# Optimization experiments

Hardware: AMD Instinct MI355X
Metric: run time of the kernel (lower is better)

Reference implementation:

```python
import jax, jax.numpy as jnp
import numpy as np

PAD_TOKEN_ID = 0
EPS = 1e-12  # torch F.normalize eps

B_Q, L_Q = 64, 32
B_D, L_D = 512, 256
HID, OUT = 768, 128
VOCAB = 30522


def setup_inputs() -> dict:
    key = jax.random.key(0)
    k1, k2, k3, k4, k5 = jax.random.split(key, 5)
    return {
        "q_hidden": jax.random.normal(k1, (B_Q, L_Q, HID), dtype=jnp.float32),
        "d_hidden": jax.random.normal(k2, (B_D, L_D, HID), dtype=jnp.float32),
        "d_input_ids": jax.random.randint(k3, (B_D, L_D), 0, VOCAB, dtype=jnp.int32),
        "skiplist": jax.random.randint(k4, (64,), 0, VOCAB, dtype=jnp.int32),
        "W": jax.random.normal(k5, (OUT, HID), dtype=jnp.float32) * (HID ** -0.5),
    }


def _l2norm(x):
    n = jnp.sqrt(jnp.sum(x * x, axis=-1, keepdims=True))
    return x / jnp.maximum(n, EPS)


def reference(q_hidden, d_hidden, d_input_ids, skiplist, W):
    # query(): linear proj + L2 normalize      (B_q, L_q, F)
    Q = _l2norm(jnp.einsum("blh,fh->blf", q_hidden, W))
    # doc(): linear proj + L2 normalize + mask (B_d, L_d, F)
    D = _l2norm(jnp.einsum("blh,fh->blf", d_hidden, W))
    is_pad = d_input_ids == PAD_TOKEN_ID
    is_punct = jnp.any(d_input_ids[..., None] == skiplist, axis=-1)
    d_mask = (~is_pad) & (~is_punct)                     # (B_d, L_d)
    D = D * d_mask[..., None].astype(D.dtype)
    # forward(): reshape to (B, N, L, F) with B = min(B_q, B_d)
    B = min(q_hidden.shape[0], d_hidden.shape[0])
    Qr = Q.reshape(B, -1, L_Q, OUT)                      # (B, 1, L_q, F)
    Dr = D.reshape(B, -1, L_D, OUT)                      # (B, N_p, L_d, F)
    Mr = d_mask.reshape(B, -1, L_D)                      # (B, N_p, L_d)
    # similarity(): cosine MaxSim, Q @ D^T with broadcast over N_p
    sim = jnp.einsum("bqf,bndf->bnqd", Qr[:, 0], Dr)     # (B, N_p, L_q, L_d)
    sim = jnp.where(Mr[:, :, None, :], sim, -jnp.inf)
    sms = jnp.max(sim, axis=-1).mean(axis=-1)            # (B, N_p)
    return sms
```

## Files before the change

### kernel.cpp

```cpp
#include <hip/hip_runtime.h>
#include <stdint.h>

typedef float  f32x4 __attribute__((ext_vector_type(4)));
typedef short  s16x8 __attribute__((ext_vector_type(8)));
typedef unsigned int u32;
typedef unsigned short u16;
typedef unsigned int u32x4 __attribute__((ext_vector_type(4)));

#define HID 768
#define OUTF 128
#define LQ 32
#define LD 256

__device__ __forceinline__ u32 pk_rna(float lo, float hi) {
    u32 a = __builtin_bit_cast(u32, lo) + 0x8000u;
    u32 b = __builtin_bit_cast(u32, hi) + 0x8000u;
    return __builtin_amdgcn_perm(b, a, 0x07060302u);
}
__device__ __forceinline__ u16 f2bf(float x) {
    return (u16)((__builtin_bit_cast(u32, x) + 0x8000u) >> 16);
}
__device__ __forceinline__ s16x8 cvt8(f32x4 lo, f32x4 hi) {
    union { u32 u[4]; s16x8 v; } ua;
    ua.u[0] = pk_rna(lo[0], lo[1]);
    ua.u[1] = pk_rna(lo[2], lo[3]);
    ua.u[2] = pk_rna(hi[0], hi[1]);
    ua.u[3] = pk_rna(hi[2], hi[3]);
    return ua.v;
}

__global__ __launch_bounds__(256) void wconv(const float* __restrict__ W,
                                             u32* __restrict__ Wb3d) {
    int t = blockIdx.x * 256 + threadIdx.x;
    int j2   = t & 3;
    int lane = (t >> 2) & 63;
    int cf   = (t >> 8) & 7;
    int kk   = t >> 11;
    int l15 = lane & 15, g4 = lane >> 4;
    int f = cf * 16 + l15;
    int k = kk * 32 + g4 * 8 + j2 * 2;
    const float* src = W + (size_t)f * HID + k;
    Wb3d[t] = pk_rna(src[0], src[1]);
}

__global__ __launch_bounds__(256) void qproj(const float* __restrict__ qh,
                                             const u16* __restrict__ Wb3,
                                             u16* __restrict__ Qb) {
    const int b = blockIdx.x;
    const int tid = threadIdx.x;
    const int w = tid >> 6, lane = tid & 63, g = lane >> 4, l15 = lane & 15;

    f32x4 acc[2][2] = {};
    const float* A0 = qh + ((size_t)b * LQ + l15) * HID + g * 8;
    const float* A1 = A0 + 16 * HID;
    const u16* Bp = Wb3 + w * 1024 + lane * 8;

    for (int kk = 0; kk < 24; ++kk) {
        f32x4 x0 = *(const f32x4*)A0;
        f32x4 x1 = *(const f32x4*)(A0 + 4);
        f32x4 y0 = *(const f32x4*)A1;
        f32x4 y1 = *(const f32x4*)(A1 + 4);
        s16x8 b0 = *(const s16x8*)(Bp);
        s16x8 b1 = *(const s16x8*)(Bp + 512);
        s16x8 a0 = cvt8(x0, x1);
        s16x8 a1 = cvt8(y0, y1);
        acc[0][0] = __builtin_amdgcn_mfma_f32_16x16x32_bf16(a0, b0, acc[0][0], 0, 0, 0);
        acc[0][1] = __builtin_amdgcn_mfma_f32_16x16x32_bf16(a0, b1, acc[0][1], 0, 0, 0);
        acc[1][0] = __builtin_amdgcn_mfma_f32_16x16x32_bf16(a1, b0, acc[1][0], 0, 0, 0);
        acc[1][1] = __builtin_amdgcn_mfma_f32_16x16x32_bf16(a1, b1, acc[1][1], 0, 0, 0);
        A0 += 32; A1 += 32; Bp += 4096;
    }

    __shared__ float part[4][32];
    __shared__ float invl[32];
#pragma unroll
    for (int rf = 0; rf < 2; ++rf)
#pragma unroll
        for (int reg = 0; reg < 4; ++reg) {
            float ss = acc[rf][0][reg] * acc[rf][0][reg] + acc[rf][1][reg] * acc[rf][1][reg];
            ss += __shfl_xor(ss, 1); ss += __shfl_xor(ss, 2);
            ss += __shfl_xor(ss, 4); ss += __shfl_xor(ss, 8);
            if (l15 == 0) part[w][rf * 16 + g * 4 + reg] = ss;
        }
    __syncthreads();
    if (tid < 32) {
        float ss = part[0][tid] + part[1][tid] + part[2][tid] + part[3][tid];
        invl[tid] = 1.f / fmaxf(sqrtf(ss), 1e-12f);
    }
    __syncthreads();
#pragma unroll
    for (int rf = 0; rf < 2; ++rf)
#pragma unroll
        for (int cf = 0; cf < 2; ++cf)
#pragma unroll
            for (int reg = 0; reg < 4; ++reg) {
                int q = rf * 16 + g * 4 + reg;
                int f = w * 32 + cf * 16 + l15;
                Qb[(size_t)b * LQ * OUTF + q * OUTF + f] = f2bf(acc[rf][cf][reg] * invl[q]);
            }
}

__global__ __launch_bounds__(512, 2) void dmax(const float* __restrict__ dh,
                                               const int* __restrict__ ids,
                                               const int* __restrict__ skiplist,
                                               const u16* __restrict__ Wb3,
                                               const u16* __restrict__ Qb,
                                               float* __restrict__ out) {
    const int bid = blockIdx.x;
    const int tid = threadIdx.x;
    const int w = tid >> 6, lane = tid & 63, g4 = lane >> 4, l15 = lane & 15;
    const int qh_ = w >> 2;

    __shared__ __align__(16) u16 stg[3][12288];
    __shared__ __align__(16) u16 outb[2][2048];
    __shared__ __align__(16) float nrm[2][16][8];
    __shared__ float wsum[8];
    __shared__ int ms[512];
    __shared__ int sk[64];

#define PADOF(v) (((v) / 192) * 1536 + (((((v) % 192)) * 8) ^ ((((v) / 192) & 7) << 4)))
    const int pad0 = PADOF(2 * tid), pad1 = PADOF(2 * tid + 1024), pad2 = PADOF(2 * tid + 2048);

    const int swz = (l15 & 7) << 4, sw45 = swz & 48, sw6 = swz & 64;
    const int aoffE = l15 * 1536 + ((g4 * 16) ^ sw45) + sw6;
    const int aoffO = l15 * 1536 + ((g4 * 16) ^ sw45) + 64 - sw6;
    const int doffE = l15 * 256 + ((g4 * 16) ^ sw45) + sw6;
    const int doffO = l15 * 256 + ((g4 * 16) ^ sw45) + 64 - sw6;

    f32x4 LA0, LA1, LA2, LA3, LA4, LA5, LB0, LB1, LB2, LB3, LB4, LB5,
          LC0, LC1, LC2, LC3, LC4, LC5;
    s16x8 Qr0, Qr1, Qr2, Qr3;
    float rmaxH[4] = {-INFINITY, -INFINITY, -INFINITY, -INFINITY};

#define SLABBASE(sab) ((const char*)dh + (size_t)(bid + (((sab) >> 4) << 8)) * 786432 \
                       + (size_t)((sab) & 15) * 49152)

#define LISSUE(sab, S) { const char* gb_ = SLABBASE(sab) + 32 * tid; \
    S##0 = *(const f32x4*)(gb_);          S##1 = *(const f32x4*)(gb_ + 16); \
    S##2 = *(const f32x4*)(gb_ + 16384);  S##3 = *(const f32x4*)(gb_ + 16400); \
    S##4 = *(const f32x4*)(gb_ + 32768);  S##5 = *(const f32x4*)(gb_ + 32784); }

#define WSTORE(P, S) { char* sb_ = (char*)&stg[P][0]; u32x4 q_; \
    q_[0] = pk_rna(S##0[0], S##0[1]); q_[1] = pk_rna(S##0[2], S##0[3]); \
    q_[2] = pk_rna(S##1[0], S##1[1]); q_[3] = pk_rna(S##1[2], S##1[3]); \
    *(u32x4*)(sb_ + pad0) = q_; \
    q_[0] = pk_rna(S##2[0], S##2[1]); q_[1] = pk_rna(S##2[2], S##2[3]); \
    q_[2] = pk_rna(S##3[0], S##3[1]); q_[3] = pk_rna(S##3[2], S##3[3]); \
    *(u32x4*)(sb_ + pad1) = q_; \
    q_[0] = pk_rna(S##4[0], S##4[1]); q_[1] = pk_rna(S##4[2], S##4[3]); \
    q_[2] = pk_rna(S##5[0], S##5[1]); q_[3] = pk_rna(S##5[2], S##5[3]); \
    *(u32x4*)(sb_ + pad2) = q_; }

#define QLOAD(doc_) { const u16* qp_ = Qb + (size_t)((bid + (doc_) * 256) >> 3) * 4096 \
                      + (qh_ * 16 + l15) * 128 + g4 * 8; \
    Qr0 = *(const s16x8*)(qp_);      Qr1 = *(const s16x8*)(qp_ + 32); \
    Qr2 = *(const s16x8*)(qp_ + 64); Qr3 = *(const s16x8*)(qp_ + 96); }

#define GEMMN(P, s_) { \
    const char* Ab_ = (const char*)&stg[P][0]; \
    u16* ob_ = &outb[(s_) & 1][0]; \
    f32x4 ac0_ = {}, ac1_ = {}; \
    _Pragma("unroll") for (int kkp = 0; kkp < 12; ++kkp) { \
        s16x8 ae_ = *(const s16x8*)(Ab_ + aoffE + kkp * 128); \
        s16x8 ao_ = *(const s16x8*)(Ab_ + aoffO + kkp * 128); \
        ac0_ = __builtin_amdgcn_mfma_f32_16x16x32_bf16(ae_, Bf[2 * kkp],     ac0_, 0, 0, 0); \
        ac1_ = __builtin_amdgcn_mfma_f32_16x16x32_bf16(ao_, Bf[2 * kkp + 1], ac1_, 0, 0, 0); \
    } \
    f32x4 aG_ = ac0_ + ac1_; \
    _Pragma("unroll") for (int rg = 0; rg < 4; ++rg) { \
        float ss_ = aG_[rg] * aG_[rg]; \
        ss_ += __shfl_xor(ss_, 1); ss_ += __shfl_xor(ss_, 2); \
        ss_ += __shfl_xor(ss_, 4); ss_ += __shfl_xor(ss_, 8); \
        if (l15 == 0) nrm[(s_) & 1][g4 * 4 + rg][w] = ss_; \
        int dr_ = g4 * 4 + rg; \
        int of_ = (dr_ * 256 + (w * 16 + l15) * 2) ^ ((dr_ & 7) << 4); \
        *(u16*)((char*)ob_ + of_) = f2bf(aG_[rg]); \
    } }

#define TAIL(sb) { \
    if ((w & 3) == 0) { \
        const char* Db_ = (const char*)&outb[(sb) & 1][0]; \
        s16x8 d0_ = *(const s16x8*)(Db_ + doffE); \
        s16x8 d1_ = *(const s16x8*)(Db_ + doffO); \
        s16x8 d2_ = *(const s16x8*)(Db_ + doffE + 128); \
        s16x8 d3_ = *(const s16x8*)(Db_ + doffO + 128); \
        f32x4 s2_ = {}; \
        s2_ = __builtin_amdgcn_mfma_f32_16x16x32_bf16(Qr0, d0_, s2_, 0, 0, 0); \
        s2_ = __builtin_amdgcn_mfma_f32_16x16x32_bf16(Qr1, d1_, s2_, 0, 0, 0); \
        s2_ = __builtin_amdgcn_mfma_f32_16x16x32_bf16(Qr2, d2_, s2_, 0, 0, 0); \
        s2_ = __builtin_amdgcn_mfma_f32_16x16x32_bf16(Qr3, d3_, s2_, 0, 0, 0); \
        f32x4 n0_ = *(const f32x4*)&nrm[(sb) & 1][l15][0]; \
        f32x4 n1_ = *(const f32x4*)&nrm[(sb) & 1][l15][4]; \
        float ssv_ = (n0_[0] + n0_[1] + n0_[2] + n0_[3]) \
                   + (n1_[0] + n1_[1] + n1_[2] + n1_[3]); \
        float inv_ = 1.f / fmaxf(sqrtf(ssv_), 1e-12f); \
        int keep_ = ms[(((sb) >> 4) << 8) + (((sb) & 15) << 4) + l15]; \
        _Pragma("unroll") for (int rg = 0; rg < 4; ++rg) { \
            float v_ = keep_ ? s2_[rg] * inv_ : -INFINITY; \
            rmaxH[rg] = fmaxf(rmaxH[rg], v_); } \
    } \
    if (((sb) & 15) == 15) { \
        if ((w & 3) == 0) { \
            float ps_ = 0.f; \
            _Pragma("unroll") for (int rg = 0; rg < 4; ++rg) { \
                float v_ = rmaxH[rg]; \
                v_ = fmaxf(v_, __shfl_xor(v_, 1)); v_ = fmaxf(v_, __shfl_xor(v_, 2)); \
                v_ = fmaxf(v_, __shfl_xor(v_, 4)); v_ = fmaxf(v_, __shfl_xor(v_, 8)); \
                ps_ += v_; rmaxH[rg] = -INFINITY; } \
            ps_ += __shfl_xor(ps_, 16); ps_ += __shfl_xor(ps_, 32); \
            if (lane == 0) wsum[w] = ps_; \
            if ((sb) == 15) { QLOAD(1); } \
        } \
        asm volatile("s_waitcnt lgkmcnt(0)" ::: "memory"); \
        __builtin_amdgcn_s_barrier(); \
        if (tid == 0) out[bid + (((sb) >> 4) << 8)] = (wsum[0] + wsum[4]) * (1.f / 32.f); \
    } }

#define SLABSTEP(s_, PG_, PW_, RN_, RW_, doIssue_, doWr_) { \
    if (doIssue_) LISSUE((s_) + 3, RN_); \
    GEMMN(PG_, s_); \
    if (doWr_) WSTORE(PW_, RW_); \
    asm volatile("s_waitcnt lgkmcnt(0)" ::: "memory"); \
    __builtin_amdgcn_s_barrier(); \
    TAIL(s_); }

    LISSUE(0, LA);
    LISSUE(1, LB);
    LISSUE(2, LC);

    s16x8 Bf[24];
#pragma unroll
    for (int kk = 0; kk < 24; ++kk)
        Bf[kk] = *(const s16x8*)(Wb3 + (size_t)(kk * 8 + w) * 512 + lane * 8);

    if (tid < 64) sk[tid] = skiplist[tid];
    asm volatile("s_waitcnt lgkmcnt(0)" ::: "memory");
    __builtin_amdgcn_s_barrier();
    {
        int d_ = tid >> 8, r_ = tid & 255;
        int id_ = ids[(size_t)(bid + d_ * 256) * 256 + r_];
        int keep_ = (id_ != 0);
#pragma unroll
        for (int j = 0; j < 64; ++j) keep_ &= (id_ != sk[j]);
        ms[tid] = keep_;
    }
    WSTORE(0, LA);
    if ((w & 3) == 0) { QLOAD(0); }
    asm volatile("s_waitcnt lgkmcnt(0)" ::: "memory");
    __builtin_amdgcn_s_barrier();

    for (int j = 0; j < 10; ++j) {
        const int s0 = 3 * j;
        SLABSTEP(s0,     0, 1, LA, LB, true,        true);
        SLABSTEP(s0 + 1, 1, 2, LB, LC, true,        true);
        SLABSTEP(s0 + 2, 2, 0, LC, LA, s0 + 5 < 32, true);
    }
    SLABSTEP(30, 0, 1, LA, LB, false, true);
    SLABSTEP(31, 1, 2, LB, LC, false, false);
}

extern "C" void kernel_launch(void* const* d_in, const int* in_sizes, int n_in,
                              void* d_out, int out_size, void* d_ws, size_t ws_size,
                              hipStream_t stream) {
    const float* q_hidden = (const float*)d_in[0];
    const float* d_hidden = (const float*)d_in[1];
    const int*   d_ids    = (const int*)d_in[2];
    const int*   skiplist = (const int*)d_in[3];
    const float* W        = (const float*)d_in[4];
    float* out = (float*)d_out;

    u16* Wb3 = (u16*)d_ws;
    u16* Qb  = (u16*)((char*)d_ws + 256 * 1024);

    wconv<<<192, 256, 0, stream>>>(W, (u32*)Wb3);
    qproj<<<64, 256, 0, stream>>>(q_hidden, Wb3, Qb);
    dmax<<<256, 512, 0, stream>>>(d_hidden, d_ids, skiplist, Wb3, Qb, out);
}
```

Measured before the change: 102.5 us.

## Specialize warps: only six warps stage doc slabs, tail warps reload Q per slab

Global-to-LDS staging of each document slab now runs on six of the eight warps, each loading eight vectors instead of six. Warps 0 and 4 do no staging and handle the MaxSim tail. The persistent Q register fragments are dropped and Q is reloaded from global memory inside every tail step. The aim is to cut register pressure and free the tail warps from staging work so the tail overlaps better with the loads. In exchange the staging load is uneven across warps and each tail step issues extra global loads for Q.

```diff
diff --git a/kernel.cpp b/kernel.cpp
--- a/kernel.cpp
+++ b/kernel.cpp
@@ -109,7 +109,9 @@
     const int bid = blockIdx.x;
     const int tid = threadIdx.x;
     const int w = tid >> 6, lane = tid & 63, g4 = lane >> 4, l15 = lane & 15;
-    const int qh_ = w >> 2;
+    const bool stg_w = (w != 0) && (w != 4);
+    const int sw = (w < 4) ? (w - 1) : (w - 2);
+    const int st = sw * 64 + lane;
 
     __shared__ __align__(16) u16 stg[3][12288];
     __shared__ __align__(16) u16 outb[2][2048];
@@ -119,7 +121,8 @@
     __shared__ int sk[64];
 
 #define PADOF(v) (((v) / 192) * 1536 + (((((v) % 192)) * 8) ^ ((((v) / 192) & 7) << 4)))
-    const int pad0 = PADOF(2 * tid), pad1 = PADOF(2 * tid + 1024), pad2 = PADOF(2 * tid + 2048);
+    const int pd0 = PADOF(2 * st), pd1 = PADOF(2 * st + 768),
+              pd2 = PADOF(2 * st + 1536), pd3 = PADOF(2 * st + 2304);
 
     const int swz = (l15 & 7) << 4, sw45 = swz & 48, sw6 = swz & 64;
     const int aoffE = l15 * 1536 + ((g4 * 16) ^ sw45) + sw6;
@@ -127,34 +130,33 @@
     const int doffE = l15 * 256 + ((g4 * 16) ^ sw45) + sw6;
     const int doffO = l15 * 256 + ((g4 * 16) ^ sw45) + 64 - sw6;
 
-    f32x4 LA0, LA1, LA2, LA3, LA4, LA5, LB0, LB1, LB2, LB3, LB4, LB5,
-          LC0, LC1, LC2, LC3, LC4, LC5;
-    s16x8 Qr0, Qr1, Qr2, Qr3;
+    f32x4 LA0, LA1, LA2, LA3, LA4, LA5, LA6, LA7,
+          LB0, LB1, LB2, LB3, LB4, LB5, LB6, LB7,
+          LC0, LC1, LC2, LC3, LC4, LC5, LC6, LC7;
     float rmaxH[4] = {-INFINITY, -INFINITY, -INFINITY, -INFINITY};
 
 #define SLABBASE(sab) ((const char*)dh + (size_t)(bid + (((sab) >> 4) << 8)) * 786432 \
                        + (size_t)((sab) & 15) * 49152)
 
-#define LISSUE(sab, S) { const char* gb_ = SLABBASE(sab) + 32 * tid; \
+#define LISSUE(sab, S) { const char* gb_ = SLABBASE(sab) + 32 * st; \
     S##0 = *(const f32x4*)(gb_);          S##1 = *(const f32x4*)(gb_ + 16); \
-    S##2 = *(const f32x4*)(gb_ + 16384);  S##3 = *(const f32x4*)(gb_ + 16400); \
-    S##4 = *(const f32x4*)(gb_ + 32768);  S##5 = *(const f32x4*)(gb_ + 32784); }
+    S##2 = *(const f32x4*)(gb_ + 12288);  S##3 = *(const f32x4*)(gb_ + 12304); \
+    S##4 = *(const f32x4*)(gb_ + 24576);  S##5 = *(const f32x4*)(gb_ + 24592); \
+    S##6 = *(const f32x4*)(gb_ + 36864);  S##7 = *(const f32x4*)(gb_ + 36880); }
 
 #define WSTORE(P, S) { char* sb_ = (char*)&stg[P][0]; u32x4 q_; \
     q_[0] = pk_rna(S##0[0], S##0[1]); q_[1] = pk_rna(S##0[2], S##0[3]); \
     q_[2] = pk_rna(S##1[0], S##1[1]); q_[3] = pk_rna(S##1[2], S##1[3]); \
-    *(u32x4*)(sb_ + pad0) = q_; \
+    *(u32x4*)(sb_ + pd0) = q_; \
     q_[0] = pk_rna(S##2[0], S##2[1]); q_[1] = pk_rna(S##2[2], S##2[3]); \
     q_[2] = pk_rna(S##3[0], S##3[1]); q_[3] = pk_rna(S##3[2], S##3[3]); \
-    *(u32x4*)(sb_ + pad1) = q_; \
+    *(u32x4*)(sb_ + pd1) = q_; \
     q_[0] = pk_rna(S##4[0], S##4[1]); q_[1] = pk_rna(S##4[2], S##4[3]); \
     q_[2] = pk_rna(S##5[0], S##5[1]); q_[3] = pk_rna(S##5[2], S##5[3]); \
-    *(u32x4*)(sb_ + pad2) = q_; }
-
-#define QLOAD(doc_) { const u16* qp_ = Qb + (size_t)((bid + (doc_) * 256) >> 3) * 4096 \
-                      + (qh_ * 16 + l15) * 128 + g4 * 8; \
-    Qr0 = *(const s16x8*)(qp_);      Qr1 = *(const s16x8*)(qp_ + 32); \
-    Qr2 = *(const s16x8*)(qp_ + 64); Qr3 = *(const s16x8*)(qp_ + 96); }
+    *(u32x4*)(sb_ + pd2) = q_; \
+    q_[0] = pk_rna(S##6[0], S##6[1]); q_[1] = pk_rna(S##6[2], S##6[3]); \
+    q_[2] = pk_rna(S##7[0], S##7[1]); q_[3] = pk_rna(S##7[2], S##7[3]); \
+    *(u32x4*)(sb_ + pd3) = q_; }
 
 #define GEMMN(P, s_) { \
     const char* Ab_ = (const char*)&stg[P][0]; \
@@ -179,6 +181,10 @@
 
 #define TAIL(sb) { \
     if ((w & 3) == 0) { \
+        const u16* qp_ = Qb + (size_t)((bid + (((sb) >> 4)) * 256) >> 3) * 4096 \
+                         + ((w >> 2) * 16 + l15) * 128 + g4 * 8; \
+        s16x8 Qr0 = *(const s16x8*)(qp_);      s16x8 Qr1 = *(const s16x8*)(qp_ + 32); \
+        s16x8 Qr2 = *(const s16x8*)(qp_ + 64); s16x8 Qr3 = *(const s16x8*)(qp_ + 96); \
         const char* Db_ = (const char*)&outb[(sb) & 1][0]; \
         s16x8 d0_ = *(const s16x8*)(Db_ + doffE); \
         s16x8 d1_ = *(const s16x8*)(Db_ + doffO); \
@@ -209,7 +215,6 @@
                 ps_ += v_; rmaxH[rg] = -INFINITY; } \
             ps_ += __shfl_xor(ps_, 16); ps_ += __shfl_xor(ps_, 32); \
             if (lane == 0) wsum[w] = ps_; \
-            if ((sb) == 15) { QLOAD(1); } \
         } \
         asm volatile("s_waitcnt lgkmcnt(0)" ::: "memory"); \
         __builtin_amdgcn_s_barrier(); \
@@ -217,16 +222,14 @@
     } }
 
 #define SLABSTEP(s_, PG_, PW_, RN_, RW_, doIssue_, doWr_) { \
-    if (doIssue_) LISSUE((s_) + 3, RN_); \
+    if (stg_w && (doIssue_)) LISSUE((s_) + 3, RN_); \
     GEMMN(PG_, s_); \
-    if (doWr_) WSTORE(PW_, RW_); \
+    if (stg_w && (doWr_)) WSTORE(PW_, RW_); \
     asm volatile("s_waitcnt lgkmcnt(0)" ::: "memory"); \
     __builtin_amdgcn_s_barrier(); \
     TAIL(s_); }
 
-    LISSUE(0, LA);
-    LISSUE(1, LB);
-    LISSUE(2, LC);
+    if (stg_w) { LISSUE(0, LA); LISSUE(1, LB); LISSUE(2, LC); }
 
     s16x8 Bf[24];
 #pragma unroll
@@ -244,8 +247,7 @@
         for (int j = 0; j < 64; ++j) keep_ &= (id_ != sk[j]);
         ms[tid] = keep_;
     }
-    WSTORE(0, LA);
-    if ((w & 3) == 0) { QLOAD(0); }
+    if (stg_w) WSTORE(0, LA);
     asm volatile("s_waitcnt lgkmcnt(0)" ::: "memory");
     __builtin_amdgcn_s_barrier();
 
```

New measurement: 137.0 us. +33.7%, slower.
